# Kernel tuning notes

Measured on AMD Instinct MI355X. Metric: run time of the kernel, lower is better.

## Reference

```python
import jax, jax.numpy as jnp
import numpy as np
import math

MODEL_DIM = 1024
BATCH = 4
SEQ = 2048


def setup_inputs() -> dict:
    key = jax.random.key(0)
    kx, kq, kk, kv = jax.random.split(key, 4)
    x = jax.random.normal(kx, (BATCH, SEQ, MODEL_DIM), dtype=jnp.float32)
    # kaiming_uniform_(W.T, a=sqrt(5)) on a square matrix -> U(-b, b) with
    # b = sqrt(6 / ((1 + 5) * fan_in)) = 1/sqrt(model_dim)
    bound = 1.0 / math.sqrt(MODEL_DIM)
    Q = jax.random.uniform(kq, (MODEL_DIM, MODEL_DIM), jnp.float32, -bound, bound)
    K = jax.random.uniform(kk, (MODEL_DIM, MODEL_DIM), jnp.float32, -bound, bound)
    V = jax.random.uniform(kv, (MODEL_DIM, MODEL_DIM), jnp.float32, -bound, bound)
    # attention_input='both' => a = model_dim => F is the full identity mask
    F = jnp.eye(MODEL_DIM, dtype=jnp.float32)
    return {"x": x, "F": F, "Q": Q, "K": K, "V": V}


def reference(x, F, Q, K, V):
    # Qx = x @ F @ Q ; Kx = x @ F @ K ; Vx = x @ V
    xF = x @ F                      # [b, s, d]
    Qx = xF @ Q                     # [b, s, d]
    Kx = xF @ K                     # [b, s, d]
    Vx = x @ V                      # [b, s, d]
    scale = 1.0 / math.sqrt(MODEL_DIM)
    attn_scores = jnp.einsum('bsd,btd->bst', Qx, Kx) * scale  # [b, s, s]
    attn_probs = jax.nn.softmax(attn_scores, axis=-1)
    out = jnp.einsum('bst,btd->bsd', attn_probs, Vx)          # [b, s, d]
    return out
```

## Files before the change

kernel.cpp:

```cpp
#include <hip/hip_runtime.h>
#include <hip/hip_bf16.h>

using bf16 = __hip_bfloat16;
typedef __bf16 bf16x8 __attribute__((ext_vector_type(8)));
typedef float f32x4 __attribute__((ext_vector_type(4)));

#define AS3(p) ((__attribute__((address_space(3))) void*)(p))
#define AS1(p) ((const __attribute__((address_space(1))) void*)(p))

template <int W> __device__ __forceinline__ void waitv() {
  asm volatile("s_waitcnt vmcnt(%0)" ::"n"(W) : "memory");
}
#define BARR __builtin_amdgcn_s_barrier()
#define LGKM0 asm volatile("s_waitcnt lgkmcnt(0)" ::: "memory")
#define SCHEDB __builtin_amdgcn_sched_barrier(0)

__global__ void cast_f32_bf16_kernel(const float* __restrict__ in,
                                     bf16* __restrict__ out, int n4) {
  int i = blockIdx.x * blockDim.x + threadIdx.x;
  if (i >= n4) return;
  float4 v = reinterpret_cast<const float4*>(in)[i];
  union { ushort4 u; bf16 h[4]; } o;
  o.h[0] = __float2bfloat16(v.x);
  o.h[1] = __float2bfloat16(v.y);
  o.h[2] = __float2bfloat16(v.z);
  o.h[3] = __float2bfloat16(v.w);
  reinterpret_cast<ushort4*>(out)[i] = o.u;
}

__global__ void transpose3_kernel(const float* __restrict__ W0,
                                  const float* __restrict__ W1,
                                  const float* __restrict__ W2,
                                  bf16* __restrict__ out) {
  __shared__ bf16 tile[32][33];
  const float* in = (blockIdx.z == 0) ? W0 : (blockIdx.z == 1) ? W1 : W2;
  out += (long)blockIdx.z * 1024 * 1024;
  int c0 = blockIdx.x * 32, r0 = blockIdx.y * 32;
  for (int i = threadIdx.y; i < 32; i += 8)
    tile[i][threadIdx.x] = (bf16)in[(long)(r0 + i) * 1024 + c0 + threadIdx.x];
  __syncthreads();
  for (int i = threadIdx.y; i < 32; i += 8)
    out[(long)(c0 + i) * 1024 + r0 + threadIdx.x] = tile[threadIdx.x][i];
}

__device__ inline void store_c(float* p, float v) { *p = v; }
__device__ inline void store_c(bf16* p, float v) { *p = __float2bfloat16(v); }

template <int MODE, typename OutT>
__global__ __launch_bounds__(512, 1) void gemm8p_kernel(
    const bf16* __restrict__ A, const bf16* __restrict__ Bt, OutT* __restrict__ C,
    int K, int lda, int ldb, int ldc, long sAb, long sBb, long sCb,
    float* __restrict__ aux, int auxStride) {
  constexpr int HALF = 128 * 64;
  constexpr int BB = 4 * HALF;
  __shared__ alignas(16) bf16 lds[2 * BB];

  A += (long)blockIdx.z * sAb;
  Bt += (long)blockIdx.z * sBb;
  C += (long)blockIdx.z * sCb;
  if (MODE != 0) aux += (long)blockIdx.z * auxStride;
  const int tm = blockIdx.y * 256, tn = blockIdx.x * 256;
  const int tid = threadIdx.x, wv = tid >> 6, lane = tid & 63;
  const int wm = wv >> 2, wn = wv & 3;
  const int lrow = lane & 15, lkc = lane >> 4;

  f32x4 acc[8][4] = {};
  bf16x8 afr[4][2], bfr[2][2][2];

  const int co0 = (lkc ^ (lrow & 7)) * 8;
  const int co1 = ((4 + lkc) ^ (lrow & 7)) * 8;
  const int arow = wm * 64 + lrow;
  const int brow = wn * 32 + lrow;

  auto stageA = [&](bf16* buf, int kt, int mh) {
#pragma unroll
    for (int i = 0; i < 2; ++i) {
      int slot = i * 512 + tid;
      int rp = slot >> 3;
      int g = (rp & 63) | (mh << 6) | ((rp >> 6) << 7);
      int cg = (slot & 7) ^ (rp & 7);
      const bf16* src = A + (long)(tm + g) * lda + kt + cg * 8;
      __builtin_amdgcn_global_load_lds(AS1(src), AS3(buf + mh * HALF + slot * 8), 16, 0, 0);
    }
  };
  auto stageB = [&](bf16* buf, int kt, int nh) {
#pragma unroll
    for (int i = 0; i < 2; ++i) {
      int slot = i * 512 + tid;
      int rp = slot >> 3;
      int g = (rp & 31) | (nh << 5) | ((rp >> 5) << 6);
      int cg = (slot & 7) ^ (rp & 7);
      const bf16* src = Bt + (long)(tn + g) * ldb + kt + cg * 8;
      __builtin_amdgcn_global_load_lds(AS1(src),
                                       AS3(buf + 2 * HALF + nh * HALF + slot * 8), 16, 0, 0);
    }
  };

#define READ_A(MH)                                                          \
  {                                                                         \
    const bf16* pa = cur + (MH) * HALF;                                     \
    _Pragma("unroll") for (int mi = 0; mi < 4; ++mi) {                      \
      afr[mi][0] = *reinterpret_cast<const bf16x8*>(pa + (arow + mi * 16) * 64 + co0); \
      afr[mi][1] = *reinterpret_cast<const bf16x8*>(pa + (arow + mi * 16) * 64 + co1); \
    }                                                                       \
  }
#define READ_B(NH)                                                          \
  {                                                                         \
    const bf16* pb = cur + 2 * HALF + (NH) * HALF;                          \
    _Pragma("unroll") for (int nj = 0; nj < 2; ++nj) {                      \
      bfr[NH][nj][0] = *reinterpret_cast<const bf16x8*>(pb + (brow + nj * 16) * 64 + co0); \
      bfr[NH][nj][1] = *reinterpret_cast<const bf16x8*>(pb + (brow + nj * 16) * 64 + co1); \
    }                                                                       \
  }
#define MFMA_PH(MH, NH)                                                     \
  __builtin_amdgcn_s_setprio(1);                                            \
  _Pragma("unroll") for (int k = 0; k < 2; ++k)                             \
      _Pragma("unroll") for (int mi = 0; mi < 4; ++mi)                      \
          _Pragma("unroll") for (int nj = 0; nj < 2; ++nj)                  \
    acc[(MH) * 4 + mi][(NH) * 2 + nj] =                                     \
        __builtin_amdgcn_mfma_f32_16x16x32_bf16(                            \
            afr[mi][k], bfr[NH][nj][k], acc[(MH) * 4 + mi][(NH) * 2 + nj],  \
            0, 0, 0);                                                       \
  __builtin_amdgcn_s_setprio(0);

  const int NT = K / 64;
  stageA(lds, 0, 0); stageB(lds, 0, 0);
  stageA(lds, 0, 1); stageB(lds, 0, 1);
  stageA(lds + BB, 64, 0); stageB(lds + BB, 64, 0);
  waitv<8>();
  BARR;

  for (int t = 0; t < NT; ++t) {
    const bf16* cur = lds + (t & 1) * BB;
    bf16* nxt = lds + ((t & 1) ^ 1) * BB;
    READ_A(0) READ_B(0)
    SCHEDB;
    if (t + 1 < NT) { stageA(nxt, (t + 1) * 64, 1); waitv<6>(); }
    else waitv<0>();
    BARR; LGKM0; SCHEDB;
    MFMA_PH(0, 0)
    SCHEDB; BARR;
    READ_B(1)
    SCHEDB;
    if (t + 1 < NT) stageB(nxt, (t + 1) * 64, 1);
    BARR; LGKM0; SCHEDB;
    MFMA_PH(0, 1)
    SCHEDB; BARR;
    READ_A(1)
    SCHEDB;
    if (t + 2 < NT) stageA(nxt == lds ? (bf16*)lds + BB : (bf16*)lds, (t + 2) * 64, 0);
    BARR; LGKM0; SCHEDB;
    MFMA_PH(1, 0)
    SCHEDB; BARR;
    if (t + 2 < NT) {
      stageB(nxt == lds ? (bf16*)lds + BB : (bf16*)lds, (t + 2) * 64, 0);
      waitv<8>();
    } else if (t + 1 < NT) {
      waitv<4>();
    }
    BARR; SCHEDB;
    MFMA_PH(1, 1)
    SCHEDB; BARR;
  }
#undef READ_A
#undef READ_B
#undef MFMA_PH

  const int crow = lkc * 4;
#pragma unroll
  for (int mh = 0; mh < 2; ++mh)
#pragma unroll
    for (int mi = 0; mi < 4; ++mi)
#pragma unroll
      for (int r = 0; r < 4; ++r) {
        const int rowm = tm + wm * 128 + mh * 64 + mi * 16 + crow + r;
        OutT* cp = C + (long)rowm * ldc + tn + wn * 64 + lrow;
        if (MODE == 0) {
#pragma unroll
          for (int nh = 0; nh < 2; ++nh)
#pragma unroll
            for (int nj = 0; nj < 2; ++nj)
              store_c(cp + nh * 32 + nj * 16, acc[mh * 4 + mi][nh * 2 + nj][r]);
        } else {
          float rs = 0.f;
#pragma unroll
          for (int nh = 0; nh < 2; ++nh)
#pragma unroll
            for (int nj = 0; nj < 2; ++nj) {
              float e = __expf(acc[mh * 4 + mi][nh * 2 + nj][r] * 0.03125f);
              rs += e;
              store_c(cp + nh * 32 + nj * 16, e);
            }
          rs += __shfl_xor(rs, 1);
          rs += __shfl_xor(rs, 2);
          rs += __shfl_xor(rs, 4);
          rs += __shfl_xor(rs, 8);
          if ((lane & 15) == 0) atomicAdd(aux + rowm, rs);
        }
      }
}

template <int BN, int MODE, typename OutT>
__global__ __launch_bounds__(512, 1) void gemm2p_kernel(
    const bf16* __restrict__ A, const bf16* __restrict__ Bt, OutT* __restrict__ C,
    int K, int lda, int ldb, int ldc, long sAb, long sBb, long sCb,
    float* __restrict__ aux, int auxStride) {
  constexpr int BM = 256, BK = 64;
  constexpr int WN = (BN == 256) ? 4 : 2;
  constexpr int MF = (BN == 256) ? 8 : 4;
  constexpr int MCH = MF / 2;
  constexpr int NLA = 4;
  constexpr int NLB = BN / 64;
  constexpr int NL = NLA + NLB;
  constexpr int BUFELEM = (BM + BN) * BK;

  __shared__ alignas(16) bf16 lds[2 * BUFELEM];

  A += (long)blockIdx.z * sAb;
  Bt += (long)blockIdx.z * sBb;
  C += (long)blockIdx.z * sCb;
  if (MODE != 0) aux += (long)blockIdx.z * auxStride;
  const int tm = blockIdx.y * BM, tn = blockIdx.x * BN;
  const int tid = threadIdx.x, wv = tid >> 6, lane = tid & 63;
  const int wm = wv / WN, wn = wv % WN;
  const int r0 = wm * (MF * 16), c0 = wn * 64;
  const int lrow = lane & 15, lkc = lane >> 4;

  f32x4 acc[MF][4] = {};

  auto stage = [&](int buf, int kt) {
    bf16* base = lds + buf * BUFELEM;
#pragma unroll
    for (int i = 0; i < NLA; ++i) {
      int slot = i * 512 + tid;
      int row = slot >> 3;
      int cg = (slot & 7) ^ (row & 7);
      const bf16* src = A + (long)(tm + row) * lda + kt + cg * 8;
      __builtin_amdgcn_global_load_lds(AS1(src), AS3(base + slot * 8), 16, 0, 0);
    }
#pragma unroll
    for (int i = 0; i < NLB; ++i) {
      int slot = i * 512 + tid;
      int row = slot >> 3;
      int cg = (slot & 7) ^ (row & 7);
      const bf16* src = Bt + (long)(tn + row) * ldb + kt + cg * 8;
      __builtin_amdgcn_global_load_lds(AS1(src), AS3(base + BM * BK + slot * 8), 16, 0, 0);
    }
  };

  stage(0, 0);
  const int NT = K / BK;
  for (int t = 0; t < NT; ++t) {
    const int cur = t & 1;
    if (t + 1 < NT) {
      stage(cur ^ 1, (t + 1) * BK);
      waitv<NL>();
    } else {
      waitv<0>();
    }
    BARR;
    SCHEDB;

    const bf16* bA = lds + cur * BUFELEM;
    const bf16* bB = bA + BM * BK;

    bf16x8 bfr[4][2];
#pragma unroll
    for (int nj = 0; nj < 4; ++nj)
#pragma unroll
      for (int k = 0; k < 2; ++k) {
        int row = c0 + nj * 16 + lrow;
        int cx = (k * 4 + lkc) ^ (row & 7);
        bfr[nj][k] = *reinterpret_cast<const bf16x8*>(bB + row * 64 + cx * 8);
      }
#pragma unroll
    for (int ph = 0; ph < 2; ++ph) {
      bf16x8 afr[MCH][2];
#pragma unroll
      for (int mi = 0; mi < MCH; ++mi)
#pragma unroll
        for (int k = 0; k < 2; ++k) {
          int row = r0 + (ph * MCH + mi) * 16 + lrow;
          int cx = (k * 4 + lkc) ^ (row & 7);
          afr[mi][k] = *reinterpret_cast<const bf16x8*>(bA + row * 64 + cx * 8);
        }
      __builtin_amdgcn_s_setprio(1);
#pragma unroll
      for (int k = 0; k < 2; ++k)
#pragma unroll
        for (int mi = 0; mi < MCH; ++mi)
#pragma unroll
          for (int nj = 0; nj < 4; ++nj)
            acc[ph * MCH + mi][nj] = __builtin_amdgcn_mfma_f32_16x16x32_bf16(
                afr[mi][k], bfr[nj][k], acc[ph * MCH + mi][nj], 0, 0, 0);
      __builtin_amdgcn_s_setprio(0);
      SCHEDB;
      BARR;
      SCHEDB;
    }
  }

  const int crow = lkc * 4;
#pragma unroll
  for (int mi = 0; mi < MF; ++mi) {
#pragma unroll
    for (int r = 0; r < 4; ++r) {
      const int rowm = tm + r0 + mi * 16 + crow + r;
      OutT* cp = C + (long)rowm * ldc + tn + c0 + lrow;
      if (MODE == 0) {
#pragma unroll
        for (int nj = 0; nj < 4; ++nj) store_c(cp + nj * 16, acc[mi][nj][r]);
      } else if (MODE == 1) {
        float rs = 0.f;
#pragma unroll
        for (int nj = 0; nj < 4; ++nj) {
          float e = __expf(acc[mi][nj][r] * 0.03125f);
          rs += e;
          store_c(cp + nj * 16, e);
        }
        rs += __shfl_xor(rs, 1);
        rs += __shfl_xor(rs, 2);
        rs += __shfl_xor(rs, 4);
        rs += __shfl_xor(rs, 8);
        if ((lane & 15) == 0) atomicAdd(aux + rowm, rs);
      } else {
        float inv = 1.0f / aux[rowm];
#pragma unroll
        for (int nj = 0; nj < 4; ++nj) store_c(cp + nj * 16, acc[mi][nj][r] * inv);
      }
    }
  }
}

extern "C" void kernel_launch(void* const* d_in, const int* in_sizes, int n_in,
                              void* d_out, int out_size, void* d_ws, size_t ws_size,
                              hipStream_t stream) {
  const float* x = (const float*)d_in[0];
  const float* Wq = (const float*)d_in[2];
  const float* Wk = (const float*)d_in[3];
  const float* Wv = (const float*)d_in[4];
  float* out = (float*)d_out;

  const long D = 1024, S = 2048, B = 4, MS = B * S;

  bf16* xb  = (bf16*)d_ws;
  bf16* Wtc = xb + MS * D;
  bf16* QKx = Wtc + 3 * D * D;
  bf16* Vxt = QKx + MS * 2 * D;
  bf16* Sc  = Vxt + MS * D;
  float* rowsum = (float*)(Sc + B * S * S);

  dim3 blk(256);
  dim3 tblk(32, 8);

  cast_f32_bf16_kernel<<<(int)(MS * D / 4 / 256), blk, 0, stream>>>(x, xb, (int)(MS * D / 4));
  transpose3_kernel<<<dim3(32, 32, 3), tblk, 0, stream>>>(Wq, Wk, Wv, Wtc);
  gemm8p_kernel<0, bf16><<<dim3(8, 32, 1), 512, 0, stream>>>(
      xb, Wtc, QKx, 1024, 1024, 1024, 2048, 0, 0, 0, nullptr, 0);
  gemm2p_kernel<128, 0, bf16><<<dim3(16, 4, 4), 512, 0, stream>>>(
      Wtc + 2 * D * D, xb, Vxt, 1024, 1024, 1024, 2048, 0, S * D, D * S, nullptr, 0);
  hipMemsetAsync(rowsum, 0, B * S * sizeof(float), stream);
  gemm8p_kernel<1, bf16><<<dim3(8, 8, 4), 512, 0, stream>>>(
      QKx, QKx + D, Sc, 1024, 2048, 2048, 2048, S * 2 * D, S * 2 * D, S * S,
      rowsum, (int)S);
  gemm2p_kernel<128, 2, float><<<dim3(8, 8, 4), 512, 0, stream>>>(
      Sc, Vxt, out, 2048, 2048, 2048, 1024, S * S, D * S, S * D,
      rowsum, (int)S);
}
```

Baseline: 168.2 us.

## Switch BN=128 GEMMs to 32x32x16 MFMA and swizzle workgroup order across XCDs

The gemm2p kernel is rewritten to use 32x32x16 bf16 MFMA with 4 accumulators of 16 floats per wave in a 2x4 wave layout. This replaces the 16x16x32 tiles, cuts the number of MFMA issues and fragment LDS reads per k-step, and changes the epilogue mapping. A block-id swizzle that groups consecutive tiles onto the same XCD is added to both GEMM kernels to improve L2 reuse. The risks are the new epilogue's scattered per-element stores, which are less coalesced than before, and possible LDS bank conflicts with the new fragment addressing.

```diff
diff --git a/kernel.cpp b/kernel.cpp
--- a/kernel.cpp
+++ b/kernel.cpp
@@ -4,6 +4,7 @@
 using bf16 = __hip_bfloat16;
 typedef __bf16 bf16x8 __attribute__((ext_vector_type(8)));
 typedef float f32x4 __attribute__((ext_vector_type(4)));
+typedef float f32x16 __attribute__((ext_vector_type(16)));
 
 #define AS3(p) ((__attribute__((address_space(3))) void*)(p))
 #define AS1(p) ((const __attribute__((address_space(1))) void*)(p))
@@ -14,6 +15,16 @@
 #define BARR __builtin_amdgcn_s_barrier()
 #define LGKM0 asm volatile("s_waitcnt lgkmcnt(0)" ::: "memory")
 #define SCHEDB __builtin_amdgcn_sched_barrier(0)
+
+__device__ __forceinline__ void swz_bid(int& bx, int& by, int& bz) {
+  const int gx = gridDim.x, gy = gridDim.y;
+  const int nwg = gx * gy * gridDim.z;
+  const int l = blockIdx.x + gx * (blockIdx.y + gy * blockIdx.z);
+  const int L = (l & 7) * (nwg >> 3) + (l >> 3);
+  bx = L % gx;
+  by = (L / gx) % gy;
+  bz = L / (gx * gy);
+}
 
 __global__ void cast_f32_bf16_kernel(const float* __restrict__ in,
                                      bf16* __restrict__ out, int n4) {
@@ -55,11 +66,13 @@
   constexpr int BB = 4 * HALF;
   __shared__ alignas(16) bf16 lds[2 * BB];
 
-  A += (long)blockIdx.z * sAb;
-  Bt += (long)blockIdx.z * sBb;
-  C += (long)blockIdx.z * sCb;
-  if (MODE != 0) aux += (long)blockIdx.z * auxStride;
-  const int tm = blockIdx.y * 256, tn = blockIdx.x * 256;
+  int bx, by, bz;
+  swz_bid(bx, by, bz);
+  A += (long)bz * sAb;
+  Bt += (long)bz * sBb;
+  C += (long)bz * sCb;
+  if (MODE != 0) aux += (long)bz * auxStride;
+  const int tm = by * 256, tn = bx * 256;
   const int tid = threadIdx.x, wv = tid >> 6, lane = tid & 63;
   const int wm = wv >> 2, wn = wv & 3;
   const int lrow = lane & 15, lkc = lane >> 4;
@@ -200,33 +213,28 @@
       }
 }
 
-template <int BN, int MODE, typename OutT>
-__global__ __launch_bounds__(512, 1) void gemm2p_kernel(
+template <int MODE, typename OutT>
+__global__ __launch_bounds__(512, 1) void gemm2p32_kernel(
     const bf16* __restrict__ A, const bf16* __restrict__ Bt, OutT* __restrict__ C,
     int K, int lda, int ldb, int ldc, long sAb, long sBb, long sCb,
-    float* __restrict__ aux, int auxStride) {
-  constexpr int BM = 256, BK = 64;
-  constexpr int WN = (BN == 256) ? 4 : 2;
-  constexpr int MF = (BN == 256) ? 8 : 4;
-  constexpr int MCH = MF / 2;
-  constexpr int NLA = 4;
-  constexpr int NLB = BN / 64;
-  constexpr int NL = NLA + NLB;
+    const float* __restrict__ aux, int auxStride) {
+  constexpr int BM = 256, BN = 128, BK = 64;
+  constexpr int NLA = 4, NLB = 2, NL = 6;
   constexpr int BUFELEM = (BM + BN) * BK;
-
   __shared__ alignas(16) bf16 lds[2 * BUFELEM];
 
-  A += (long)blockIdx.z * sAb;
-  Bt += (long)blockIdx.z * sBb;
-  C += (long)blockIdx.z * sCb;
-  if (MODE != 0) aux += (long)blockIdx.z * auxStride;
-  const int tm = blockIdx.y * BM, tn = blockIdx.x * BN;
+  int bx, by, bz;
+  swz_bid(bx, by, bz);
+  A += (long)bz * sAb;
+  Bt += (long)bz * sBb;
+  C += (long)bz * sCb;
+  if (MODE != 0) aux += (long)bz * auxStride;
+  const int tm = by * BM, tn = bx * BN;
   const int tid = threadIdx.x, wv = tid >> 6, lane = tid & 63;
-  const int wm = wv / WN, wn = wv % WN;
-  const int r0 = wm * (MF * 16), c0 = wn * 64;
-  const int lrow = lane & 15, lkc = lane >> 4;
-
-  f32x4 acc[MF][4] = {};
+  const int wm = wv >> 2, wn = wv & 3;
+  const int lcol = lane & 31, khalf = lane >> 5;
+
+  f32x16 acc[4] = {};
 
   auto stage = [&](int buf, int kt) {
     bf16* base = lds + buf * BUFELEM;
@@ -247,6 +255,9 @@
       __builtin_amdgcn_global_load_lds(AS1(src), AS3(base + BM * BK + slot * 8), 16, 0, 0);
     }
   };
+
+  const int arow0 = wm * 128 + lcol;
+  const int brow = wn * 32 + lcol;
 
   stage(0, 0);
   const int NT = K / BK;
@@ -264,35 +275,30 @@
     const bf16* bA = lds + cur * BUFELEM;
     const bf16* bB = bA + BM * BK;
 
-    bf16x8 bfr[4][2];
-#pragma unroll
-    for (int nj = 0; nj < 4; ++nj)
-#pragma unroll
-      for (int k = 0; k < 2; ++k) {
-        int row = c0 + nj * 16 + lrow;
-        int cx = (k * 4 + lkc) ^ (row & 7);
-        bfr[nj][k] = *reinterpret_cast<const bf16x8*>(bB + row * 64 + cx * 8);
-      }
+    bf16x8 bfr[4];
+#pragma unroll
+    for (int kk = 0; kk < 4; ++kk) {
+      int cx = (kk * 2 + khalf) ^ (brow & 7);
+      bfr[kk] = *reinterpret_cast<const bf16x8*>(bB + brow * 64 + cx * 8);
+    }
 #pragma unroll
     for (int ph = 0; ph < 2; ++ph) {
-      bf16x8 afr[MCH][2];
-#pragma unroll
-      for (int mi = 0; mi < MCH; ++mi)
-#pragma unroll
-        for (int k = 0; k < 2; ++k) {
-          int row = r0 + (ph * MCH + mi) * 16 + lrow;
-          int cx = (k * 4 + lkc) ^ (row & 7);
-          afr[mi][k] = *reinterpret_cast<const bf16x8*>(bA + row * 64 + cx * 8);
+      bf16x8 afr[4][2];
+#pragma unroll
+      for (int mi = 0; mi < 4; ++mi)
+#pragma unroll
+        for (int j = 0; j < 2; ++j) {
+          int ra = arow0 + mi * 32;
+          int cx = ((ph * 2 + j) * 2 + khalf) ^ (ra & 7);
+          afr[mi][j] = *reinterpret_cast<const bf16x8*>(bA + ra * 64 + cx * 8);
         }
       __builtin_amdgcn_s_setprio(1);
 #pragma unroll
-      for (int k = 0; k < 2; ++k)
-#pragma unroll
-        for (int mi = 0; mi < MCH; ++mi)
-#pragma unroll
-          for (int nj = 0; nj < 4; ++nj)
-            acc[ph * MCH + mi][nj] = __builtin_amdgcn_mfma_f32_16x16x32_bf16(
-                afr[mi][k], bfr[nj][k], acc[ph * MCH + mi][nj], 0, 0, 0);
+      for (int j = 0; j < 2; ++j)
+#pragma unroll
+        for (int mi = 0; mi < 4; ++mi)
+          acc[mi] = __builtin_amdgcn_mfma_f32_32x32x16_bf16(
+              afr[mi][j], bfr[ph * 2 + j], acc[mi], 0, 0, 0);
       __builtin_amdgcn_s_setprio(0);
       SCHEDB;
       BARR;
@@ -300,36 +306,17 @@
     }
   }
 
-  const int crow = lkc * 4;
-#pragma unroll
-  for (int mi = 0; mi < MF; ++mi) {
-#pragma unroll
-    for (int r = 0; r < 4; ++r) {
-      const int rowm = tm + r0 + mi * 16 + crow + r;
-      OutT* cp = C + (long)rowm * ldc + tn + c0 + lrow;
-      if (MODE == 0) {
-#pragma unroll
-        for (int nj = 0; nj < 4; ++nj) store_c(cp + nj * 16, acc[mi][nj][r]);
-      } else if (MODE == 1) {
-        float rs = 0.f;
-#pragma unroll
-        for (int nj = 0; nj < 4; ++nj) {
-          float e = __expf(acc[mi][nj][r] * 0.03125f);
-          rs += e;
-          store_c(cp + nj * 16, e);
-        }
-        rs += __shfl_xor(rs, 1);
-        rs += __shfl_xor(rs, 2);
-        rs += __shfl_xor(rs, 4);
-        rs += __shfl_xor(rs, 8);
-        if ((lane & 15) == 0) atomicAdd(aux + rowm, rs);
-      } else {
-        float inv = 1.0f / aux[rowm];
-#pragma unroll
-        for (int nj = 0; nj < 4; ++nj) store_c(cp + nj * 16, acc[mi][nj][r] * inv);
-      }
-    }
-  }
+#pragma unroll
+  for (int mi = 0; mi < 4; ++mi)
+#pragma unroll
+    for (int r = 0; r < 16; ++r) {
+      const int row = (r & 3) + 8 * (r >> 2) + 4 * khalf;
+      const int rowm = tm + wm * 128 + mi * 32 + row;
+      OutT* cp = C + (long)rowm * ldc + tn + wn * 32 + lcol;
+      float v = acc[mi][r];
+      if (MODE == 2) v *= 1.0f / aux[rowm];
+      store_c(cp, v);
+    }
 }
 
 extern "C" void kernel_launch(void* const* d_in, const int* in_sizes, int n_in,
@@ -357,13 +344,13 @@
   transpose3_kernel<<<dim3(32, 32, 3), tblk, 0, stream>>>(Wq, Wk, Wv, Wtc);
   gemm8p_kernel<0, bf16><<<dim3(8, 32, 1), 512, 0, stream>>>(
       xb, Wtc, QKx, 1024, 1024, 1024, 2048, 0, 0, 0, nullptr, 0);
-  gemm2p_kernel<128, 0, bf16><<<dim3(16, 4, 4), 512, 0, stream>>>(
+  gemm2p32_kernel<0, bf16><<<dim3(16, 4, 4), 512, 0, stream>>>(
       Wtc + 2 * D * D, xb, Vxt, 1024, 1024, 1024, 2048, 0, S * D, D * S, nullptr, 0);
   hipMemsetAsync(rowsum, 0, B * S * sizeof(float), stream);
   gemm8p_kernel<1, bf16><<<dim3(8, 8, 4), 512, 0, stream>>>(
       QKx, QKx + D, Sc, 1024, 2048, 2048, 2048, S * 2 * D, S * 2 * D, S * S,
       rowsum, (int)S);
-  gemm2p_kernel<128, 2, float><<<dim3(8, 8, 4), 512, 0, stream>>>(
+  gemm2p32_kernel<2, float><<<dim3(8, 8, 4), 512, 0, stream>>>(
       Sc, Vxt, out, 2048, 2048, 2048, 1024, S * S, D * S, S * D,
       rowsum, (int)S);
 }
```

Measured after the change: 173.0 us. +2.9%, slower.
